# Performance work log

Measured on AMD Instinct MI355X. Metric: run time of the kernel, lower is better.

## Reference

```python
import jax, jax.numpy as jnp
import numpy as np

B, S, E, H, Dh = 1, 2048, 1024, 16, 64


def setup_inputs() -> dict:
    key = jax.random.key(0)
    ks = jax.random.split(key, 9)
    sc = 0.02
    return {
        "x": jax.random.normal(ks[0], (B, S, E), jnp.float32),
        "Wq": jax.random.normal(ks[1], (H, E, Dh), jnp.float32) * sc,
        "bq": jax.random.normal(ks[2], (H, Dh), jnp.float32) * sc,
        "Wk": jax.random.normal(ks[3], (H, E, Dh), jnp.float32) * sc,
        "bk": jax.random.normal(ks[4], (H, Dh), jnp.float32) * sc,
        "Wv": jax.random.normal(ks[5], (H, E, Dh), jnp.float32) * sc,
        "bv": jax.random.normal(ks[6], (H, Dh), jnp.float32) * sc,
        "Wo": jax.random.normal(ks[7], (E, E), jnp.float32) * sc,
        "bo": jax.random.normal(ks[8], (E,), jnp.float32) * sc,
    }


def reference(x, Wq, bq, Wk, bk, Wv, bv, Wo, bo):
    # Per-head projections (stacked): [B,S,E] x [H,E,Dh] -> [B,H,S,Dh]
    q = jnp.einsum("bse,hed->bhsd", x, Wq) + bq[None, :, None, :]
    k = jnp.einsum("bse,hed->bhsd", x, Wk) + bk[None, :, None, :]
    v = jnp.einsum("bse,hed->bhsd", x, Wv) + bv[None, :, None, :]
    scores = jnp.einsum("bhsd,bhtd->bhst", q, k) / np.sqrt(Dh).astype(np.float32)
    causal = jnp.tril(jnp.ones((S, S), dtype=bool))  # [S,S]
    scores = jnp.where(causal[None, None], scores, -jnp.inf)
    attn = jax.nn.softmax(scores, axis=-1)  # attn_dropout p=0 -> identity
    out = jnp.einsum("bhst,bhtd->bhsd", attn, v)
    # concat heads in head order: [B,S,H*Dh]
    out = out.transpose(0, 2, 1, 3).reshape(B, S, H * Dh)
    return out @ Wo.T if False else jnp.einsum("bsf,ef->bse", out, Wo.T.T * 0 + Wo) if False else out @ Wo.swapaxes(0, 1) * 0 + (jnp.einsum("bsf,fe->bse", out, Wo) + bo)
```

## Files before the change

kernel.cpp:

```cpp
#include <hip/hip_runtime.h>
#include <hip/hip_bf16.h>

#define S_LEN 2048
#define E_DIM 1024
#define NH 16
#define DH 64

typedef __bf16 v8bf __attribute__((ext_vector_type(8)));
typedef float f32x4 __attribute__((ext_vector_type(4)));
typedef unsigned short u16x4 __attribute__((ext_vector_type(4)));
typedef unsigned short u16x8 __attribute__((ext_vector_type(8)));

__device__ __align__(16) unsigned short g_Xb[S_LEN * E_DIM];
__device__ __align__(16) unsigned short g_WT[3 * E_DIM * E_DIM];
__device__ __align__(16) unsigned short g_WoT[E_DIM * E_DIM];
__device__ __align__(16) unsigned short g_Qb[NH * S_LEN * DH];
__device__ __align__(16) unsigned short g_Kb[NH * S_LEN * DH];
__device__ __align__(16) unsigned short g_Vt[NH * DH * S_LEN];
__device__ __align__(16) unsigned short g_AO[S_LEN * E_DIM];

__device__ inline unsigned short f2bf(float f) {
    unsigned int u = __float_as_uint(f);
    u += 0x7FFF + ((u >> 16) & 1);
    return (unsigned short)(u >> 16);
}
__device__ inline f32x4 mfma16(v8bf a, v8bf b, f32x4 c) {
    return __builtin_amdgcn_mfma_f32_16x16x32_bf16(a, b, c, 0, 0, 0);
}

typedef __attribute__((address_space(3))) unsigned int lds_u32;
typedef __attribute__((address_space(1))) const unsigned int glb_u32;
__device__ inline void async_cp16(const unsigned short* g, unsigned short* l) {
    __builtin_amdgcn_global_load_lds((glb_u32*)g, (lds_u32*)l, 16, 0, 0);
}

__global__ __launch_bounds__(256) void prep(const float* __restrict__ X,
                                            const float* __restrict__ Wq,
                                            const float* __restrict__ Wk,
                                            const float* __restrict__ Wv,
                                            const float* __restrict__ Wo) {
    __shared__ __align__(16) unsigned short lds[64 * 72];
    const int b = blockIdx.x;
    const int t = threadIdx.x;
    if (b < 2048) {
        int i = b * 256 + t;
        f32x4 v = reinterpret_cast<const f32x4*>(X)[i];
        u16x4 o = {f2bf(v.x), f2bf(v.y), f2bf(v.z), f2bf(v.w)};
        reinterpret_cast<u16x4*>(g_Xb)[i] = o;
    } else if (b < 2304) {
        int bb = b - 2048;
        const int h = bb >> 4;
        const int e0 = (bb & 15) * 64;
        const float* srcs[3] = {Wq, Wk, Wv};
#pragma unroll
        for (int tn = 0; tn < 3; tn++) {
            const float* W = srcs[tn] + h * 65536;
#pragma unroll
            for (int p = 0; p < 4; p++) {
                int e = p * 16 + (t >> 4);
                int d = (t & 15) * 4;
                f32x4 v = *reinterpret_cast<const f32x4*>(&W[(e0 + e) * 64 + d]);
                lds[(d + 0) * 72 + e] = f2bf(v.x);
                lds[(d + 1) * 72 + e] = f2bf(v.y);
                lds[(d + 2) * 72 + e] = f2bf(v.z);
                lds[(d + 3) * 72 + e] = f2bf(v.w);
            }
            __syncthreads();
#pragma unroll
            for (int p = 0; p < 2; p++) {
                int d = p * 32 + (t >> 3);
                int ec = (t & 7) * 8;
                u16x8 o = *reinterpret_cast<const u16x8*>(&lds[d * 72 + ec]);
                *reinterpret_cast<u16x8*>(&g_WT[(tn * 1024 + h * 64 + d) * E_DIM + e0 + ec]) = o;
            }
            __syncthreads();
        }
    } else {
        int bb = b - 2304;
        const int f0 = (bb >> 4) * 64;
        const int e0 = (bb & 15) * 64;
#pragma unroll
        for (int p = 0; p < 4; p++) {
            int f = p * 16 + (t >> 4);
            int e = (t & 15) * 4;
            f32x4 v = *reinterpret_cast<const f32x4*>(&Wo[(f0 + f) * E_DIM + e0 + e]);
            lds[(e + 0) * 72 + f] = f2bf(v.x);
            lds[(e + 1) * 72 + f] = f2bf(v.y);
            lds[(e + 2) * 72 + f] = f2bf(v.z);
            lds[(e + 3) * 72 + f] = f2bf(v.w);
        }
        __syncthreads();
#pragma unroll
        for (int p = 0; p < 2; p++) {
            int e = p * 32 + (t >> 3);
            int fc = (t & 7) * 8;
            u16x8 o = *reinterpret_cast<const u16x8*>(&lds[e * 72 + fc]);
            *reinterpret_cast<u16x8*>(&g_WoT[(e0 + e) * E_DIM + f0 + fc]) = o;
        }
    }
}

__global__ __launch_bounds__(256) void qkv_gemm(const float* __restrict__ bq,
                                                const float* __restrict__ bk,
                                                const float* __restrict__ bv) {
    __shared__ __align__(16) unsigned short lds[12288];
    unsigned short* lA = lds;
    unsigned short* lB = lds + 8192;
    const int t = threadIdx.x;
    const int wave = t >> 6;
    const int lane = t & 63;
    const int m = lane & 15, quad = lane >> 4;
    const int s0 = blockIdx.x * 128;
    const int n0 = blockIdx.y * 64;

    const int rl = t >> 3;
    const int cx = (t & 7) ^ (rl & 7);
    const int axor = m & 7;

    f32x4 acc[2][4];
#pragma unroll
    for (int i = 0; i < 2; i++)
#pragma unroll
        for (int j = 0; j < 4; j++) acc[i][j] = (f32x4){0.f, 0.f, 0.f, 0.f};

    const unsigned short* lAr0 = lA + (wave * 32 + m) * 64;
    const unsigned short* lAr1 = lA + (wave * 32 + 16 + m) * 64;

    for (int k0 = 0; k0 < E_DIM; k0 += 64) {
        const unsigned short* ga = g_Xb + (s0 + rl) * E_DIM + k0 + cx * 8;
        async_cp16(ga,              lA + wave * 512);
        async_cp16(ga + 32 * E_DIM, lA + 2048 + wave * 512);
        async_cp16(ga + 64 * E_DIM, lA + 4096 + wave * 512);
        async_cp16(ga + 96 * E_DIM, lA + 6144 + wave * 512);
        const unsigned short* gb = g_WT + (n0 + rl) * E_DIM + k0 + cx * 8;
        async_cp16(gb,              lB + wave * 512);
        async_cp16(gb + 32 * E_DIM, lB + 2048 + wave * 512);
        __syncthreads();
#pragma unroll
        for (int ks = 0; ks < 2; ks++) {
            const int ch = ((ks * 4 + quad) ^ axor) * 8;
            v8bf a0 = *reinterpret_cast<const v8bf*>(lAr0 + ch);
            v8bf a1 = *reinterpret_cast<const v8bf*>(lAr1 + ch);
#pragma unroll
            for (int j = 0; j < 4; j++) {
                v8bf bfr = *reinterpret_cast<const v8bf*>(lB + (j * 16 + m) * 64 + ch);
                acc[0][j] = mfma16(a0, bfr, acc[0][j]);
                acc[1][j] = mfma16(a1, bfr, acc[1][j]);
            }
        }
        __syncthreads();
    }

    const int tensor = n0 >> 10;
    const int nn0 = n0 & 1023;
    const int hh = nn0 >> 6;
    const float* bb = tensor == 0 ? bq : (tensor == 1 ? bk : bv);
    float bias[4];
#pragma unroll
    for (int j = 0; j < 4; j++) bias[j] = bb[nn0 + j * 16 + m];

    if (tensor < 2) {
#pragma unroll
        for (int i = 0; i < 2; i++)
#pragma unroll
            for (int j = 0; j < 4; j++)
#pragma unroll
                for (int r = 0; r < 4; r++) {
                    int sl = wave * 32 + i * 16 + quad * 4 + r;
                    int nl = j * 16 + m;
                    lds[sl * 72 + nl] = f2bf(acc[i][j][r] + bias[j]);
                }
        __syncthreads();
        unsigned short* dst = (tensor == 0 ? g_Qb : g_Kb) + (hh * S_LEN + s0) * DH;
#pragma unroll
        for (int p = 0; p < 4; p++) {
            int row = p * 32 + (t >> 3);
            int c = t & 7;
            u16x8 v = *reinterpret_cast<const u16x8*>(&lds[row * 72 + c * 8]);
            *reinterpret_cast<u16x8*>(&dst[row * DH + c * 8]) = v;
        }
    } else {
#pragma unroll
        for (int i = 0; i < 2; i++)
#pragma unroll
            for (int j = 0; j < 4; j++)
#pragma unroll
                for (int r = 0; r < 4; r++) {
                    int sl = wave * 32 + i * 16 + quad * 4 + r;
                    int nl = j * 16 + m;
                    lds[nl * 136 + sl] = f2bf(acc[i][j][r] + bias[j]);
                }
        __syncthreads();
#pragma unroll
        for (int p = 0; p < 4; p++) {
            int nl = p * 16 + (t >> 4);
            int sc = t & 15;
            u16x8 v = *reinterpret_cast<const u16x8*>(&lds[nl * 136 + sc * 8]);
            *reinterpret_cast<u16x8*>(&g_Vt[(hh * DH + nl) * S_LEN + s0 + sc * 8]) = v;
        }
    }
}

__global__ __launch_bounds__(256) void flash_attn() {
    __shared__ __align__(16) unsigned char smem[24576];
    unsigned short* plds = (unsigned short*)smem;
    float* comb = (float*)smem;
    const int t = threadIdx.x;
    const int wave = t >> 6, lane = t & 63;
    const int m = lane & 15, quad = lane >> 4;
    const int h = blockIdx.x & 15;
    const int Tp = blockIdx.x >> 4;
    const int qq = Tp >> 4, tt = Tp & 15;
    const int T = (qq == 0) ? tt : (qq == 1) ? 31 - tt : (qq == 2) ? 32 + tt : 63 - tt;
    const int s0 = T * 32;

    const unsigned short* Qh = g_Qb + h * S_LEN * DH;
    const unsigned short* Kh = g_Kb + h * S_LEN * DH;
    const unsigned short* Vh = g_Vt + h * DH * S_LEN;

    v8bf aqA0 = *reinterpret_cast<const v8bf*>(Qh + (s0 + m) * DH + quad * 8);
    v8bf aqA1 = *reinterpret_cast<const v8bf*>(Qh + (s0 + m) * DH + 32 + quad * 8);
    v8bf aqB0 = *reinterpret_cast<const v8bf*>(Qh + (s0 + 16 + m) * DH + quad * 8);
    v8bf aqB1 = *reinterpret_cast<const v8bf*>(Qh + (s0 + 16 + m) * DH + 32 + quad * 8);

    f32x4 oA[4], oB[4];
#pragma unroll
    for (int i = 0; i < 4; i++) { oA[i] = (f32x4){0.f,0.f,0.f,0.f}; oB[i] = (f32x4){0.f,0.f,0.f,0.f}; }
    f32x4 laccA = (f32x4){0.f,0.f,0.f,0.f}, laccB = (f32x4){0.f,0.f,0.f,0.f};

    v8bf ones;
#pragma unroll
    for (int i = 0; i < 8; i++) ones[i] = (__bf16)1.0f;

    const float SC = 0.125f * 1.44269504088896f;
    unsigned short* pw = plds + wave * 2304;
    const int tEnd = s0 + 32;

    int t0 = wave * 64;
    v8bf kf[4][2];
    if (t0 < tEnd) {
#pragma unroll
        for (int ct = 0; ct < 4; ct++) {
            const unsigned short* kp = Kh + (t0 + ct * 16 + m) * DH + quad * 8;
            kf[ct][0] = *reinterpret_cast<const v8bf*>(kp);
            kf[ct][1] = *reinterpret_cast<const v8bf*>(kp + 32);
        }
    }

    for (; t0 < tEnd; t0 += 256) {
        const bool doA = (t0 < s0 + 16);
        const int t1 = t0 + 256;

        v8bf vf[4][2];
#pragma unroll
        for (int dt = 0; dt < 4; dt++) {
            const unsigned short* vp = Vh + (dt * 16 + m) * S_LEN + t0 + quad * 8;
            vf[dt][0] = *reinterpret_cast<const v8bf*>(vp);
            vf[dt][1] = *reinterpret_cast<const v8bf*>(vp + 32);
        }

        f32x4 sB[4];
#pragma unroll
        for (int ct = 0; ct < 4; ct++) {
            sB[ct] = (f32x4){0.f,0.f,0.f,0.f};
            sB[ct] = mfma16(aqB0, kf[ct][0], sB[ct]);
            sB[ct] = mfma16(aqB1, kf[ct][1], sB[ct]);
        }
        f32x4 sA[4];
        if (doA) {
#pragma unroll
            for (int ct = 0; ct < 4; ct++) {
                sA[ct] = (f32x4){0.f,0.f,0.f,0.f};
                sA[ct] = mfma16(aqA0, kf[ct][0], sA[ct]);
                sA[ct] = mfma16(aqA1, kf[ct][1], sA[ct]);
            }
        }

        v8bf kfn[4][2];
        if (t1 < tEnd) {
#pragma unroll
            for (int ct = 0; ct < 4; ct++) {
                const unsigned short* kp = Kh + (t1 + ct * 16 + m) * DH + quad * 8;
                kfn[ct][0] = *reinterpret_cast<const v8bf*>(kp);
                kfn[ct][1] = *reinterpret_cast<const v8bf*>(kp + 32);
            }
        }

#pragma unroll
        for (int ct = 0; ct < 4; ct++) {
            int colbase = t0 + ct * 16;
            int col = colbase + m;
            if (colbase + 15 > s0 + 16) {
#pragma unroll
                for (int r = 0; r < 4; r++)
                    if (col > s0 + 16 + quad * 4 + r) sB[ct][r] = -3e38f;
            }
            if (doA && colbase + 15 > s0) {
#pragma unroll
                for (int r = 0; r < 4; r++)
                    if (col > s0 + quad * 4 + r) sA[ct][r] = -3e38f;
            }
        }

#pragma unroll
        for (int ct = 0; ct < 4; ct++) {
#pragma unroll
            for (int r = 0; r < 4; r++)
                sB[ct][r] = __builtin_amdgcn_exp2f(sB[ct][r] * SC);
            __hip_bfloat162 p01 = __float22bfloat162_rn(make_float2(sB[ct][0], sB[ct][1]));
            __hip_bfloat162 p23 = __float22bfloat162_rn(make_float2(sB[ct][2], sB[ct][3]));
            unsigned short* pb = pw + (16 + quad * 4) * 72 + ct * 16 + m;
            pb[0]   = *reinterpret_cast<unsigned short*>(&p01.x);
            pb[72]  = *reinterpret_cast<unsigned short*>(&p01.y);
            pb[144] = *reinterpret_cast<unsigned short*>(&p23.x);
            pb[216] = *reinterpret_cast<unsigned short*>(&p23.y);
        }
        if (doA) {
#pragma unroll
            for (int ct = 0; ct < 4; ct++) {
#pragma unroll
                for (int r = 0; r < 4; r++)
                    sA[ct][r] = __builtin_amdgcn_exp2f(sA[ct][r] * SC);
                __hip_bfloat162 p01 = __float22bfloat162_rn(make_float2(sA[ct][0], sA[ct][1]));
                __hip_bfloat162 p23 = __float22bfloat162_rn(make_float2(sA[ct][2], sA[ct][3]));
                unsigned short* pa = pw + (quad * 4) * 72 + ct * 16 + m;
                pa[0]   = *reinterpret_cast<unsigned short*>(&p01.x);
                pa[72]  = *reinterpret_cast<unsigned short*>(&p01.y);
                pa[144] = *reinterpret_cast<unsigned short*>(&p23.x);
                pa[216] = *reinterpret_cast<unsigned short*>(&p23.y);
            }
        }
        __builtin_amdgcn_s_waitcnt(0xC07F);
        v8bf apB0 = *reinterpret_cast<const v8bf*>(pw + (16 + m) * 72 + quad * 8);
        v8bf apB1 = *reinterpret_cast<const v8bf*>(pw + (16 + m) * 72 + 32 + quad * 8);
#pragma unroll
        for (int dt = 0; dt < 4; dt++) {
            oB[dt] = mfma16(apB0, vf[dt][0], oB[dt]);
            oB[dt] = mfma16(apB1, vf[dt][1], oB[dt]);
        }
        laccB = mfma16(apB0, ones, laccB);
        laccB = mfma16(apB1, ones, laccB);
        if (doA) {
            v8bf apA0 = *reinterpret_cast<const v8bf*>(pw + m * 72 + quad * 8);
            v8bf apA1 = *reinterpret_cast<const v8bf*>(pw + m * 72 + 32 + quad * 8);
#pragma unroll
            for (int dt = 0; dt < 4; dt++) {
                oA[dt] = mfma16(apA0, vf[dt][0], oA[dt]);
                oA[dt] = mfma16(apA1, vf[dt][1], oA[dt]);
            }
            laccA = mfma16(apA0, ones, laccA);
            laccA = mfma16(apA1, ones, laccA);
        }
        if (t1 < tEnd) {
#pragma unroll
            for (int ct = 0; ct < 4; ct++) {
                kf[ct][0] = kfn[ct][0];
                kf[ct][1] = kfn[ct][1];
            }
        }
    }

    float* cw = comb + (wave * 64 + lane) * 24;
    __syncthreads();
#pragma unroll
    for (int dt = 0; dt < 4; dt++) *reinterpret_cast<f32x4*>(cw + dt * 4) = oA[dt];
    *reinterpret_cast<f32x4*>(cw + 16) = laccA;
    __syncthreads();
    {
        f32x4 oAt = (f32x4){0.f,0.f,0.f,0.f}, l4 = (f32x4){0.f,0.f,0.f,0.f};
#pragma unroll
        for (int w = 0; w < 4; w++) {
            const float* cr = comb + (w * 64 + lane) * 24;
            oAt += *reinterpret_cast<const f32x4*>(cr + wave * 4);
            l4  += *reinterpret_cast<const f32x4*>(cr + 16);
        }
#pragma unroll
        for (int r = 0; r < 4; r++) {
            float inv = 1.0f / l4[r];
            g_AO[(s0 + quad * 4 + r) * E_DIM + h * 64 + wave * 16 + m] = f2bf(oAt[r] * inv);
        }
    }
    __syncthreads();
#pragma unroll
    for (int dt = 0; dt < 4; dt++) *reinterpret_cast<f32x4*>(cw + dt * 4) = oB[dt];
    *reinterpret_cast<f32x4*>(cw + 16) = laccB;
    __syncthreads();
    {
        f32x4 oBt = (f32x4){0.f,0.f,0.f,0.f}, l4 = (f32x4){0.f,0.f,0.f,0.f};
#pragma unroll
        for (int w = 0; w < 4; w++) {
            const float* cr = comb + (w * 64 + lane) * 24;
            oBt += *reinterpret_cast<const f32x4*>(cr + wave * 4);
            l4  += *reinterpret_cast<const f32x4*>(cr + 16);
        }
#pragma unroll
        for (int r = 0; r < 4; r++) {
            float inv = 1.0f / l4[r];
            g_AO[(s0 + 16 + quad * 4 + r) * E_DIM + h * 64 + wave * 16 + m] = f2bf(oBt[r] * inv);
        }
    }
}

__global__ __launch_bounds__(256) void out_gemm(const float* __restrict__ bo,
                                                float* __restrict__ OUT) {
    __shared__ __align__(16) unsigned short lds[8192];
    unsigned short* lA = lds;
    unsigned short* lB = lds + 4096;
    const int t = threadIdx.x;
    const int wave = t >> 6;
    const int lane = t & 63;
    const int m = lane & 15, quad = lane >> 4;
    const int wr = (wave >> 1) * 32, wc = (wave & 1) * 32;
    const int s0 = blockIdx.x * 64;
    const int n0 = blockIdx.y * 64;

    const int rl = t >> 3;
    const int cx = (t & 7) ^ (rl & 7);
    const int axor = m & 7;

    f32x4 acc[2][2];
#pragma unroll
    for (int i = 0; i < 2; i++)
#pragma unroll
        for (int j = 0; j < 2; j++) acc[i][j] = (f32x4){0.f, 0.f, 0.f, 0.f};

    for (int k0 = 0; k0 < E_DIM; k0 += 64) {
        const unsigned short* ga = g_AO + (s0 + rl) * E_DIM + k0 + cx * 8;
        async_cp16(ga,              lA + wave * 512);
        async_cp16(ga + 32 * E_DIM, lA + 2048 + wave * 512);
        const unsigned short* gb = g_WoT + (n0 + rl) * E_DIM + k0 + cx * 8;
        async_cp16(gb,              lB + wave * 512);
        async_cp16(gb + 32 * E_DIM, lB + 2048 + wave * 512);
        __syncthreads();
#pragma unroll
        for (int ks = 0; ks < 2; ks++) {
            const int ch = ((ks * 4 + quad) ^ axor) * 8;
            v8bf a0 = *reinterpret_cast<const v8bf*>(lA + (wr + m) * 64 + ch);
            v8bf a1 = *reinterpret_cast<const v8bf*>(lA + (wr + 16 + m) * 64 + ch);
#pragma unroll
            for (int j = 0; j < 2; j++) {
                v8bf bfr = *reinterpret_cast<const v8bf*>(lB + (wc + j * 16 + m) * 64 + ch);
                acc[0][j] = mfma16(a0, bfr, acc[0][j]);
                acc[1][j] = mfma16(a1, bfr, acc[1][j]);
            }
        }
        __syncthreads();
    }
#pragma unroll
    for (int i = 0; i < 2; i++)
#pragma unroll
        for (int j = 0; j < 2; j++) {
            int e = n0 + wc + j * 16 + m;
            float bias = bo[e];
#pragma unroll
            for (int r = 0; r < 4; r++) {
                int s = s0 + wr + i * 16 + quad * 4 + r;
                OUT[s * E_DIM + e] = acc[i][j][r] + bias;
            }
        }
}

extern "C" void kernel_launch(void* const* d_in, const int* in_sizes, int n_in,
                              void* d_out, int out_size, void* d_ws, size_t ws_size,
                              hipStream_t stream) {
    (void)in_sizes; (void)n_in; (void)out_size; (void)d_ws; (void)ws_size;
    const float* x  = (const float*)d_in[0];
    const float* Wq = (const float*)d_in[1];
    const float* bq = (const float*)d_in[2];
    const float* Wk = (const float*)d_in[3];
    const float* bk = (const float*)d_in[4];
    const float* Wv = (const float*)d_in[5];
    const float* bv = (const float*)d_in[6];
    const float* Wo = (const float*)d_in[7];
    const float* bo = (const float*)d_in[8];
    float* out = (float*)d_out;

    hipLaunchKernelGGL(prep,       dim3(2560),   dim3(256), 0, stream, x, Wq, Wk, Wv, Wo);
    hipLaunchKernelGGL(qkv_gemm,   dim3(16, 48), dim3(256), 0, stream, bq, bk, bv);
    hipLaunchKernelGGL(flash_attn, dim3(1024),   dim3(256), 0, stream);
    hipLaunchKernelGGL(out_gemm,   dim3(32, 16), dim3(256), 0, stream, bo, out);
}
```

Baseline: 165.2 us.

## Double-buffer GEMM LDS loads, reorder flash-attn loop with prefetch and priority

The QKV and output GEMMs now double-buffer their LDS tiles, so the async copy of the next K-slice is issued before computing on the current one. The output GEMM also moves to 128-row tiles with 4 column fragments per wave, which halves the grid. The flash attention loop prefetches the next K and V fragments in registers, does the B-half PV MFMAs before the A-half softmax, and wraps MFMA sections in s_setprio, with launch bounds asking for 3 blocks per CU. The aim is to hide global-memory latency and raise MFMA utilisation, at the cost of more LDS per block (lower occupancy) and fewer output-GEMM blocks.

```diff
diff --git a/kernel.cpp b/kernel.cpp
--- a/kernel.cpp
+++ b/kernel.cpp
@@ -103,9 +103,7 @@
 __global__ __launch_bounds__(256) void qkv_gemm(const float* __restrict__ bq,
                                                 const float* __restrict__ bk,
                                                 const float* __restrict__ bv) {
-    __shared__ __align__(16) unsigned short lds[12288];
-    unsigned short* lA = lds;
-    unsigned short* lB = lds + 8192;
+    __shared__ __align__(16) unsigned short lds[24576];
     const int t = threadIdx.x;
     const int wave = t >> 6;
     const int lane = t & 63;
@@ -123,19 +121,31 @@
 #pragma unroll
         for (int j = 0; j < 4; j++) acc[i][j] = (f32x4){0.f, 0.f, 0.f, 0.f};
 
-    const unsigned short* lAr0 = lA + (wave * 32 + m) * 64;
-    const unsigned short* lAr1 = lA + (wave * 32 + 16 + m) * 64;
-
-    for (int k0 = 0; k0 < E_DIM; k0 += 64) {
-        const unsigned short* ga = g_Xb + (s0 + rl) * E_DIM + k0 + cx * 8;
+    const unsigned short* gA = g_Xb + (s0 + rl) * E_DIM + cx * 8;
+    const unsigned short* gB = g_WT + (n0 + rl) * E_DIM + cx * 8;
+
+    auto stage = [&](int k0, int buf) {
+        unsigned short* lA = lds + buf * 12288;
+        unsigned short* lB = lA + 8192;
+        const unsigned short* ga = gA + k0;
         async_cp16(ga,              lA + wave * 512);
         async_cp16(ga + 32 * E_DIM, lA + 2048 + wave * 512);
         async_cp16(ga + 64 * E_DIM, lA + 4096 + wave * 512);
         async_cp16(ga + 96 * E_DIM, lA + 6144 + wave * 512);
-        const unsigned short* gb = g_WT + (n0 + rl) * E_DIM + k0 + cx * 8;
+        const unsigned short* gb = gB + k0;
         async_cp16(gb,              lB + wave * 512);
         async_cp16(gb + 32 * E_DIM, lB + 2048 + wave * 512);
-        __syncthreads();
+    };
+
+    stage(0, 0);
+    __syncthreads();
+    int buf = 0;
+    for (int k0 = 0; k0 < E_DIM; k0 += 64) {
+        if (k0 + 64 < E_DIM) stage(k0 + 64, buf ^ 1);
+        const unsigned short* lA = lds + buf * 12288;
+        const unsigned short* lB = lA + 8192;
+        const unsigned short* lAr0 = lA + (wave * 32 + m) * 64;
+        const unsigned short* lAr1 = lAr0 + 16 * 64;
 #pragma unroll
         for (int ks = 0; ks < 2; ks++) {
             const int ch = ((ks * 4 + quad) ^ axor) * 8;
@@ -149,6 +159,7 @@
             }
         }
         __syncthreads();
+        buf ^= 1;
     }
 
     const int tensor = n0 >> 10;
@@ -201,7 +212,7 @@
     }
 }
 
-__global__ __launch_bounds__(256) void flash_attn() {
+__global__ __launch_bounds__(256, 3) void flash_attn() {
     __shared__ __align__(16) unsigned char smem[24576];
     unsigned short* plds = (unsigned short*)smem;
     float* comb = (float*)smem;
@@ -237,7 +248,7 @@
     const int tEnd = s0 + 32;
 
     int t0 = wave * 64;
-    v8bf kf[4][2];
+    v8bf kf[4][2], vf[4][2];
     if (t0 < tEnd) {
 #pragma unroll
         for (int ct = 0; ct < 4; ct++) {
@@ -245,20 +256,19 @@
             kf[ct][0] = *reinterpret_cast<const v8bf*>(kp);
             kf[ct][1] = *reinterpret_cast<const v8bf*>(kp + 32);
         }
-    }
-
-    for (; t0 < tEnd; t0 += 256) {
-        const bool doA = (t0 < s0 + 16);
-        const int t1 = t0 + 256;
-
-        v8bf vf[4][2];
 #pragma unroll
         for (int dt = 0; dt < 4; dt++) {
             const unsigned short* vp = Vh + (dt * 16 + m) * S_LEN + t0 + quad * 8;
             vf[dt][0] = *reinterpret_cast<const v8bf*>(vp);
             vf[dt][1] = *reinterpret_cast<const v8bf*>(vp + 32);
         }
-
+    }
+
+    for (; t0 < tEnd; t0 += 256) {
+        const bool doA = (t0 < s0 + 16);
+        const int t1 = t0 + 256;
+
+        __builtin_amdgcn_s_setprio(1);
         f32x4 sB[4];
 #pragma unroll
         for (int ct = 0; ct < 4; ct++) {
@@ -275,14 +285,14 @@
                 sA[ct] = mfma16(aqA1, kf[ct][1], sA[ct]);
             }
         }
-
-        v8bf kfn[4][2];
+        __builtin_amdgcn_s_setprio(0);
+
         if (t1 < tEnd) {
 #pragma unroll
             for (int ct = 0; ct < 4; ct++) {
                 const unsigned short* kp = Kh + (t1 + ct * 16 + m) * DH + quad * 8;
-                kfn[ct][0] = *reinterpret_cast<const v8bf*>(kp);
-                kfn[ct][1] = *reinterpret_cast<const v8bf*>(kp + 32);
+                kf[ct][0] = *reinterpret_cast<const v8bf*>(kp);
+                kf[ct][1] = *reinterpret_cast<const v8bf*>(kp + 32);
             }
         }
 
@@ -295,13 +305,7 @@
                 for (int r = 0; r < 4; r++)
                     if (col > s0 + 16 + quad * 4 + r) sB[ct][r] = -3e38f;
             }
-            if (doA && colbase + 15 > s0) {
-#pragma unroll
-                for (int r = 0; r < 4; r++)
-                    if (col > s0 + quad * 4 + r) sA[ct][r] = -3e38f;
-            }
-        }
-
+        }
 #pragma unroll
         for (int ct = 0; ct < 4; ct++) {
 #pragma unroll
@@ -315,7 +319,32 @@
             pb[144] = *reinterpret_cast<unsigned short*>(&p23.x);
             pb[216] = *reinterpret_cast<unsigned short*>(&p23.y);
         }
+        __builtin_amdgcn_s_waitcnt(0xC07F);
+        {
+            v8bf apB0 = *reinterpret_cast<const v8bf*>(pw + (16 + m) * 72 + quad * 8);
+            v8bf apB1 = *reinterpret_cast<const v8bf*>(pw + (16 + m) * 72 + 32 + quad * 8);
+            __builtin_amdgcn_s_setprio(1);
+#pragma unroll
+            for (int dt = 0; dt < 4; dt++) {
+                oB[dt] = mfma16(apB0, vf[dt][0], oB[dt]);
+                oB[dt] = mfma16(apB1, vf[dt][1], oB[dt]);
+            }
+            laccB = mfma16(apB0, ones, laccB);
+            laccB = mfma16(apB1, ones, laccB);
+            __builtin_amdgcn_s_setprio(0);
+        }
+
         if (doA) {
+#pragma unroll
+            for (int ct = 0; ct < 4; ct++) {
+                int colbase = t0 + ct * 16;
+                int col = colbase + m;
+                if (colbase + 15 > s0) {
+#pragma unroll
+                    for (int r = 0; r < 4; r++)
+                        if (col > s0 + quad * 4 + r) sA[ct][r] = -3e38f;
+                }
+            }
 #pragma unroll
             for (int ct = 0; ct < 4; ct++) {
 #pragma unroll
@@ -329,20 +358,10 @@
                 pa[144] = *reinterpret_cast<unsigned short*>(&p23.x);
                 pa[216] = *reinterpret_cast<unsigned short*>(&p23.y);
             }
-        }
-        __builtin_amdgcn_s_waitcnt(0xC07F);
-        v8bf apB0 = *reinterpret_cast<const v8bf*>(pw + (16 + m) * 72 + quad * 8);
-        v8bf apB1 = *reinterpret_cast<const v8bf*>(pw + (16 + m) * 72 + 32 + quad * 8);
-#pragma unroll
-        for (int dt = 0; dt < 4; dt++) {
-            oB[dt] = mfma16(apB0, vf[dt][0], oB[dt]);
-            oB[dt] = mfma16(apB1, vf[dt][1], oB[dt]);
-        }
-        laccB = mfma16(apB0, ones, laccB);
-        laccB = mfma16(apB1, ones, laccB);
-        if (doA) {
+            __builtin_amdgcn_s_waitcnt(0xC07F);
             v8bf apA0 = *reinterpret_cast<const v8bf*>(pw + m * 72 + quad * 8);
             v8bf apA1 = *reinterpret_cast<const v8bf*>(pw + m * 72 + 32 + quad * 8);
+            __builtin_amdgcn_s_setprio(1);
 #pragma unroll
             for (int dt = 0; dt < 4; dt++) {
                 oA[dt] = mfma16(apA0, vf[dt][0], oA[dt]);
@@ -350,12 +369,15 @@
             }
             laccA = mfma16(apA0, ones, laccA);
             laccA = mfma16(apA1, ones, laccA);
-        }
+            __builtin_amdgcn_s_setprio(0);
+        }
+
         if (t1 < tEnd) {
 #pragma unroll
-            for (int ct = 0; ct < 4; ct++) {
-                kf[ct][0] = kfn[ct][0];
-                kf[ct][1] = kfn[ct][1];
+            for (int dt = 0; dt < 4; dt++) {
+                const unsigned short* vp = Vh + (dt * 16 + m) * S_LEN + t1 + quad * 8;
+                vf[dt][0] = *reinterpret_cast<const v8bf*>(vp);
+                vf[dt][1] = *reinterpret_cast<const v8bf*>(vp + 32);
             }
         }
     }
@@ -403,58 +425,73 @@
 
 __global__ __launch_bounds__(256) void out_gemm(const float* __restrict__ bo,
                                                 float* __restrict__ OUT) {
-    __shared__ __align__(16) unsigned short lds[8192];
-    unsigned short* lA = lds;
-    unsigned short* lB = lds + 4096;
+    __shared__ __align__(16) unsigned short lds[24576];
     const int t = threadIdx.x;
     const int wave = t >> 6;
     const int lane = t & 63;
     const int m = lane & 15, quad = lane >> 4;
-    const int wr = (wave >> 1) * 32, wc = (wave & 1) * 32;
-    const int s0 = blockIdx.x * 64;
+    const int s0 = blockIdx.x * 128;
     const int n0 = blockIdx.y * 64;
 
     const int rl = t >> 3;
     const int cx = (t & 7) ^ (rl & 7);
     const int axor = m & 7;
 
-    f32x4 acc[2][2];
+    f32x4 acc[2][4];
 #pragma unroll
     for (int i = 0; i < 2; i++)
 #pragma unroll
-        for (int j = 0; j < 2; j++) acc[i][j] = (f32x4){0.f, 0.f, 0.f, 0.f};
-
-    for (int k0 = 0; k0 < E_DIM; k0 += 64) {
-        const unsigned short* ga = g_AO + (s0 + rl) * E_DIM + k0 + cx * 8;
+        for (int j = 0; j < 4; j++) acc[i][j] = (f32x4){0.f, 0.f, 0.f, 0.f};
+
+    const unsigned short* gA = g_AO + (s0 + rl) * E_DIM + cx * 8;
+    const unsigned short* gB = g_WoT + (n0 + rl) * E_DIM + cx * 8;
+
+    auto stage = [&](int k0, int buf) {
+        unsigned short* lA = lds + buf * 12288;
+        unsigned short* lB = lA + 8192;
+        const unsigned short* ga = gA + k0;
         async_cp16(ga,              lA + wave * 512);
         async_cp16(ga + 32 * E_DIM, lA + 2048 + wave * 512);
-        const unsigned short* gb = g_WoT + (n0 + rl) * E_DIM + k0 + cx * 8;
+        async_cp16(ga + 64 * E_DIM, lA + 4096 + wave * 512);
+        async_cp16(ga + 96 * E_DIM, lA + 6144 + wave * 512);
+        const unsigned short* gb = gB + k0;
         async_cp16(gb,              lB + wave * 512);
         async_cp16(gb + 32 * E_DIM, lB + 2048 + wave * 512);
-        __syncthreads();
+    };
+
+    stage(0, 0);
+    __syncthreads();
+    int buf = 0;
+    for (int k0 = 0; k0 < E_DIM; k0 += 64) {
+        if (k0 + 64 < E_DIM) stage(k0 + 64, buf ^ 1);
+        const unsigned short* lA = lds + buf * 12288;
+        const unsigned short* lB = lA + 8192;
+        const unsigned short* lAr0 = lA + (wave * 32 + m) * 64;
+        const unsigned short* lAr1 = lAr0 + 16 * 64;
 #pragma unroll
         for (int ks = 0; ks < 2; ks++) {
             const int ch = ((ks * 4 + quad) ^ axor) * 8;
-            v8bf a0 = *reinterpret_cast<const v8bf*>(lA + (wr + m) * 64 + ch);
-            v8bf a1 = *reinterpret_cast<const v8bf*>(lA + (wr + 16 + m) * 64 + ch);
-#pragma unroll
-            for (int j = 0; j < 2; j++) {
-                v8bf bfr = *reinterpret_cast<const v8bf*>(lB + (wc + j * 16 + m) * 64 + ch);
+            v8bf a0 = *reinterpret_cast<const v8bf*>(lAr0 + ch);
+            v8bf a1 = *reinterpret_cast<const v8bf*>(lAr1 + ch);
+#pragma unroll
+            for (int j = 0; j < 4; j++) {
+                v8bf bfr = *reinterpret_cast<const v8bf*>(lB + (j * 16 + m) * 64 + ch);
                 acc[0][j] = mfma16(a0, bfr, acc[0][j]);
                 acc[1][j] = mfma16(a1, bfr, acc[1][j]);
             }
         }
         __syncthreads();
+        buf ^= 1;
     }
 #pragma unroll
     for (int i = 0; i < 2; i++)
 #pragma unroll
-        for (int j = 0; j < 2; j++) {
-            int e = n0 + wc + j * 16 + m;
+        for (int j = 0; j < 4; j++) {
+            int e = n0 + j * 16 + m;
             float bias = bo[e];
 #pragma unroll
             for (int r = 0; r < 4; r++) {
-                int s = s0 + wr + i * 16 + quad * 4 + r;
+                int s = s0 + wave * 32 + i * 16 + quad * 4 + r;
                 OUT[s * E_DIM + e] = acc[i][j][r] + bias;
             }
         }
@@ -478,5 +515,5 @@
     hipLaunchKernelGGL(prep,       dim3(2560),   dim3(256), 0, stream, x, Wq, Wk, Wv, Wo);
     hipLaunchKernelGGL(qkv_gemm,   dim3(16, 48), dim3(256), 0, stream, bq, bk, bv);
     hipLaunchKernelGGL(flash_attn, dim3(1024),   dim3(256), 0, stream);
-    hipLaunchKernelGGL(out_gemm,   dim3(32, 16), dim3(256), 0, stream, bo, out);
-}
+    hipLaunchKernelGGL(out_gemm,   dim3(16, 16), dim3(256), 0, stream, bo, out);
+}
```

New measurement: 195.2 us. 1.18x slower.
